# Kernel tuning notes

Hardware: AMD Instinct MI355X
Metric: run time of the kernel (lower is better)

## Reference

```python
import jax, jax.numpy as jnp
import numpy as np

_MIN_BLOCK_KV = 32


def setup_inputs() -> dict:
    key = jax.random.key(0)
    k0, k1, k2, k3 = jax.random.split(key, 4)
    B, H, HKV, D, T, S = 32, 32, 8, 128, 2048, 8
    pool = B * T
    q = jax.random.normal(k0, (B, H, D), dtype=jnp.float32)
    k_buffer = jax.random.normal(k1, (pool, HKV, D), dtype=jnp.float32)
    v_buffer = jax.random.normal(k2, (pool, HKV, D), dtype=jnp.float32)
    # uniform contexts: request b owns tokens [b*T, (b+1)*T) of the pool, in permuted (paged) order
    kv_indptr = (jnp.arange(B + 1, dtype=jnp.int32) * T)
    kv_indices = jax.random.permutation(k3, pool).astype(jnp.int32)
    num_kv_splits = jnp.full((B,), S, dtype=jnp.int32)
    return {"q": q, "k_buffer": k_buffer, "v_buffer": v_buffer,
            "kv_indptr": kv_indptr, "kv_indices": kv_indices,
            "num_kv_splits": num_kv_splits}


def reference(q, k_buffer, v_buffer, kv_indptr, kv_indices, num_kv_splits):
    # Paged KV-cache decode attention, stage 1 (split-KV partial softmax).
    B, H, D = q.shape
    HKV = k_buffer.shape[1]
    Lv = v_buffer.shape[-1]
    G = H // HKV                       # GQA group size
    sm_scale = 1.0 / (D ** 0.5)        # Model default (sm_scale=None)
    logit_cap = 0.0                    # Model default -> capping disabled

    seq_lens = kv_indptr[1:] - kv_indptr[:-1]          # [B]
    T = kv_indices.shape[0] // B                       # max context len (uniform setup)
    S = int(jnp.max(num_kv_splits))                    # max_kv_splits (eager, as in torch code)

    pos = jnp.arange(T, dtype=jnp.int32)               # [T]
    valid = pos[None, :] < seq_lens[:, None]           # [B,T]
    # gather KV pool locations per (batch, position); clamp OOB positions
    gidx = kv_indptr[:-1, None] + jnp.minimum(pos[None, :], seq_lens[:, None] - 1)
    kv_loc = kv_indices[gidx]                          # [B,T]
    k_g = k_buffer[kv_loc]                             # [B,T,HKV,D]
    v_g = v_buffer[kv_loc]                             # [B,T,HKV,Lv]

    qr = q.reshape(B, HKV, G, D)
    qk = jnp.einsum('bkgd,btkd->bkgt', qr, k_g) * sm_scale   # [B,HKV,G,T]
    if logit_cap > 0:
        qk = logit_cap * jnp.tanh(qk / logit_cap)

    # split assignment: kv_len_per_split = cdiv(cdiv(seq_len, splits), MIN) * MIN
    cdiv = lambda a, b: (a + b - 1) // b
    kv_len_per_split = cdiv(cdiv(seq_lens, num_kv_splits), _MIN_BLOCK_KV) * _MIN_BLOCK_KV  # [B]
    split_id = pos[None, :] // kv_len_per_split[:, None]      # [B,T]
    split_mask = (split_id[:, None, :] == jnp.arange(S, dtype=jnp.int32)[None, :, None]) \
                 & valid[:, None, :]                          # [B,S,T]

    neg_inf = jnp.float32(-jnp.inf)
    masked = jnp.where(split_mask[:, None, None, :, :], qk[:, :, :, None, :], neg_inf)  # [B,HKV,G,S,T]
    m = jnp.max(masked, axis=-1)                               # [B,HKV,G,S]
    m_safe = jnp.where(jnp.isfinite(m), m, 0.0)                # guard empty splits
    p = jnp.exp(masked - m_safe[..., None])                    # [B,HKV,G,S,T]
    p = jnp.where(split_mask[:, None, None, :, :], p, 0.0)
    e_sum = jnp.sum(p, axis=-1)                                # [B,HKV,G,S]
    acc = jnp.einsum('bkgst,btkv->bkgsv', p, v_g)              # [B,HKV,G,S,Lv]

    att_out = (acc / e_sum[..., None]).reshape(B, H, S, Lv)
    att_lse = (m + jnp.log(e_sum)).reshape(B, H, S)
    return att_out, att_lse
```

## Files before the change

### kernel.cpp

```cpp
#include <hip/hip_runtime.h>
#include <math.h>


namespace {
constexpr int kB = 32;
constexpr int kH = 32;
constexpr int kHKV = 8;
constexpr int kD = 128;
constexpr int kG = kH / kHKV;
constexpr int kS = 8;
constexpr int kMinBlockKV = 32;
}

__global__ __launch_bounds__(256, 8) void decode_split_kernel(
    const float* __restrict__ q,
    const float* __restrict__ k_buffer,
    const float* __restrict__ v_buffer,
    const int* __restrict__ kv_indptr,
    const int* __restrict__ kv_indices,
    const int* __restrict__ num_kv_splits,
    float* __restrict__ att_out,
    float* __restrict__ att_lse)
{
    const int bid = blockIdx.x;
    const int s  = bid % kS;
    const int kh = (bid / kS) % kHKV;
    const int b  = bid / (kS * kHKV);

    const int tid  = threadIdx.x;
    const int wave = tid >> 6;
    const int lane = tid & 63;

    const int ptr0    = kv_indptr[b];
    const int seq_len = kv_indptr[b + 1] - ptr0;
    const int splits  = num_kv_splits[b];
    const int per     = (seq_len + splits - 1) / splits;
    const int lps     = ((per + kMinBlockKV - 1) / kMinBlockKV) * kMinBlockKV;
    const int t0 = s * lps;
    const int t1 = min(t0 + lps, seq_len);

    const float sm_scale = 0.08838834764831845f;

    float2 qv[kG];
    const float* qbase = q + ((size_t)b * kH + (size_t)kh * kG) * kD + lane * 2;
    #pragma unroll
    for (int g = 0; g < kG; ++g) {
        float2 t = *(const float2*)(qbase + (size_t)g * kD);
        qv[g].x = t.x * sm_scale;
        qv[g].y = t.y * sm_scale;
    }

    float  l[kG]   = {0.f, 0.f, 0.f, 0.f};
    float2 acc[kG];
    #pragma unroll
    for (int g = 0; g < kG; ++g) acc[g] = make_float2(0.f, 0.f);

    for (int base = t0 + wave * 64; base < t1; base += 256) {
        const int nt = min(64, t1 - base);
        int my_loc = 0;
        if (lane < nt) my_loc = kv_indices[ptr0 + base + lane];

        for (int tt = 0; tt < nt; ++tt) {
            const int loc = __shfl(my_loc, tt);
            const float* krow = k_buffer + ((size_t)loc * kHKV + kh) * kD + lane * 2;
            const float* vrow = v_buffer + ((size_t)loc * kHKV + kh) * kD + lane * 2;
            const float2 kk = *(const float2*)krow;
            const float2 vv = *(const float2*)vrow;

            float dot[kG];
            #pragma unroll
            for (int g = 0; g < kG; ++g)
                dot[g] = qv[g].x * kk.x + qv[g].y * kk.y;
            #pragma unroll
            for (int m = 32; m >= 1; m >>= 1) {
                #pragma unroll
                for (int g = 0; g < kG; ++g)
                    dot[g] += __shfl_xor(dot[g], m);
            }
            #pragma unroll
            for (int g = 0; g < kG; ++g) {
                const float p = __expf(dot[g]);
                l[g] += p;
                acc[g].x += p * vv.x;
                acc[g].y += p * vv.y;
            }
        }
    }

    __shared__ float s_acc[4][kG][kD];
    __shared__ float s_l[4][kG];
    #pragma unroll
    for (int g = 0; g < kG; ++g)
        *(float2*)&s_acc[wave][g][lane * 2] = acc[g];
    if (lane == 0) {
        #pragma unroll
        for (int g = 0; g < kG; ++g) s_l[wave][g] = l[g];
    }
    __syncthreads();

    const int g = tid >> 6;
    const int d = (tid & 63) * 2;
    float a0 = 0.f, a1 = 0.f, ls = 0.f;
    #pragma unroll
    for (int w = 0; w < 4; ++w) {
        a0 += s_acc[w][g][d];
        a1 += s_acc[w][g][d + 1];
        ls += s_l[w][g];
    }
    const float inv = 1.0f / ls;
    const size_t hidx = (size_t)b * kH + (size_t)kh * kG + g;
    float* outp = att_out + (hidx * kS + s) * kD + d;
    outp[0] = a0 * inv;
    outp[1] = a1 * inv;
    if ((tid & 63) == 0)
        att_lse[hidx * kS + s] = logf(ls);
}

extern "C" void kernel_launch(void* const* d_in, const int* in_sizes, int n_in,
                              void* d_out, int out_size, void* d_ws, size_t ws_size,
                              hipStream_t stream) {
    const float* q             = (const float*)d_in[0];
    const float* k_buffer      = (const float*)d_in[1];
    const float* v_buffer      = (const float*)d_in[2];
    const int*   kv_indptr     = (const int*)d_in[3];
    const int*   kv_indices    = (const int*)d_in[4];
    const int*   num_kv_splits = (const int*)d_in[5];

    float* att_out = (float*)d_out;
    float* att_lse = att_out + (size_t)kB * kH * kS * kD;

    dim3 grid(kB * kHKV * kS);
    decode_split_kernel<<<grid, 256, 0, stream>>>(
        q, k_buffer, v_buffer, kv_indptr, kv_indices, num_kv_splits,
        att_out, att_lse);
}
```

Before: 555.5 us.

## Process four tokens per wave with float4 loads and register prefetch

```diff
diff --git a/kernel.cpp b/kernel.cpp
--- a/kernel.cpp
+++ b/kernel.cpp
@@ -12,7 +12,7 @@
 constexpr int kMinBlockKV = 32;
 }
 
-__global__ __launch_bounds__(256, 8) void decode_split_kernel(
+__global__ __launch_bounds__(256, 4) void decode_split_kernel(
     const float* __restrict__ q,
     const float* __restrict__ k_buffer,
     const float* __restrict__ v_buffer,
@@ -30,6 +30,8 @@
     const int tid  = threadIdx.x;
     const int wave = tid >> 6;
     const int lane = tid & 63;
+    const int tg   = lane >> 4;
+    const int li   = lane & 15;
 
     const int ptr0    = kv_indptr[b];
     const int seq_len = kv_indptr[b + 1] - ptr0;
@@ -41,77 +43,136 @@
 
     const float sm_scale = 0.08838834764831845f;
 
-    float2 qv[kG];
-    const float* qbase = q + ((size_t)b * kH + (size_t)kh * kG) * kD + lane * 2;
+    float4 q0[kG], q1[kG];
+    const float* qb = q + ((size_t)b * kH + (size_t)kh * kG) * kD;
     #pragma unroll
     for (int g = 0; g < kG; ++g) {
-        float2 t = *(const float2*)(qbase + (size_t)g * kD);
-        qv[g].x = t.x * sm_scale;
-        qv[g].y = t.y * sm_scale;
+        float4 a = *(const float4*)(qb + (size_t)g * kD + li * 4);
+        float4 c = *(const float4*)(qb + (size_t)g * kD + 64 + li * 4);
+        q0[g] = make_float4(a.x * sm_scale, a.y * sm_scale, a.z * sm_scale, a.w * sm_scale);
+        q1[g] = make_float4(c.x * sm_scale, c.y * sm_scale, c.z * sm_scale, c.w * sm_scale);
     }
 
-    float  l[kG]   = {0.f, 0.f, 0.f, 0.f};
-    float2 acc[kG];
+    float  l[kG] = {0.f, 0.f, 0.f, 0.f};
+    float4 a0[kG], a1[kG];
     #pragma unroll
-    for (int g = 0; g < kG; ++g) acc[g] = make_float2(0.f, 0.f);
+    for (int g = 0; g < kG; ++g) {
+        a0[g] = make_float4(0.f, 0.f, 0.f, 0.f);
+        a1[g] = make_float4(0.f, 0.f, 0.f, 0.f);
+    }
 
     for (int base = t0 + wave * 64; base < t1; base += 256) {
         const int nt = min(64, t1 - base);
         int my_loc = 0;
         if (lane < nt) my_loc = kv_indices[ptr0 + base + lane];
+        const int ng = (nt + 3) >> 2;
 
-        for (int tt = 0; tt < nt; ++tt) {
-            const int loc = __shfl(my_loc, tt);
-            const float* krow = k_buffer + ((size_t)loc * kHKV + kh) * kD + lane * 2;
-            const float* vrow = v_buffer + ((size_t)loc * kHKV + kh) * kD + lane * 2;
-            const float2 kk = *(const float2*)krow;
-            const float2 vv = *(const float2*)vrow;
+        int loc = __shfl(my_loc, min(tg, nt - 1));
+        const float* kb = k_buffer + ((size_t)loc * kHKV + kh) * kD;
+        const float* vb = v_buffer + ((size_t)loc * kHKV + kh) * kD;
+        float4 ck0 = *(const float4*)(kb + li * 4);
+        float4 ck1 = *(const float4*)(kb + 64 + li * 4);
+        float4 cv0 = *(const float4*)(vb + li * 4);
+        float4 cv1 = *(const float4*)(vb + 64 + li * 4);
+
+        for (int ig = 0; ig < ng; ++ig) {
+            float4 nk0, nk1, nv0, nv1;
+            const bool have_next = (ig + 1 < ng);
+            if (have_next) {
+                const int idx = (ig + 1) * 4 + tg;
+                const int loc2 = __shfl(my_loc, min(idx, nt - 1));
+                const float* kb2 = k_buffer + ((size_t)loc2 * kHKV + kh) * kD;
+                const float* vb2 = v_buffer + ((size_t)loc2 * kHKV + kh) * kD;
+                nk0 = *(const float4*)(kb2 + li * 4);
+                nk1 = *(const float4*)(kb2 + 64 + li * 4);
+                nv0 = *(const float4*)(vb2 + li * 4);
+                nv1 = *(const float4*)(vb2 + 64 + li * 4);
+            }
 
             float dot[kG];
             #pragma unroll
-            for (int g = 0; g < kG; ++g)
-                dot[g] = qv[g].x * kk.x + qv[g].y * kk.y;
+            for (int g = 0; g < kG; ++g) {
+                float d = q0[g].x * ck0.x;
+                d = fmaf(q0[g].y, ck0.y, d);
+                d = fmaf(q0[g].z, ck0.z, d);
+                d = fmaf(q0[g].w, ck0.w, d);
+                d = fmaf(q1[g].x, ck1.x, d);
+                d = fmaf(q1[g].y, ck1.y, d);
+                d = fmaf(q1[g].z, ck1.z, d);
+                d = fmaf(q1[g].w, ck1.w, d);
+                dot[g] = d;
+            }
             #pragma unroll
-            for (int m = 32; m >= 1; m >>= 1) {
+            for (int m = 1; m <= 8; m <<= 1) {
                 #pragma unroll
                 for (int g = 0; g < kG; ++g)
                     dot[g] += __shfl_xor(dot[g], m);
             }
+
+            const bool valid = (ig * 4 + tg) < nt;
             #pragma unroll
             for (int g = 0; g < kG; ++g) {
-                const float p = __expf(dot[g]);
+                const float p = valid ? __expf(dot[g]) : 0.f;
                 l[g] += p;
-                acc[g].x += p * vv.x;
-                acc[g].y += p * vv.y;
+                a0[g].x = fmaf(p, cv0.x, a0[g].x);
+                a0[g].y = fmaf(p, cv0.y, a0[g].y);
+                a0[g].z = fmaf(p, cv0.z, a0[g].z);
+                a0[g].w = fmaf(p, cv0.w, a0[g].w);
+                a1[g].x = fmaf(p, cv1.x, a1[g].x);
+                a1[g].y = fmaf(p, cv1.y, a1[g].y);
+                a1[g].z = fmaf(p, cv1.z, a1[g].z);
+                a1[g].w = fmaf(p, cv1.w, a1[g].w);
             }
+
+            if (have_next) { ck0 = nk0; ck1 = nk1; cv0 = nv0; cv1 = nv1; }
+        }
+    }
+
+    #pragma unroll
+    for (int m = 16; m <= 32; m <<= 1) {
+        #pragma unroll
+        for (int g = 0; g < kG; ++g) {
+            a0[g].x += __shfl_xor(a0[g].x, m);
+            a0[g].y += __shfl_xor(a0[g].y, m);
+            a0[g].z += __shfl_xor(a0[g].z, m);
+            a0[g].w += __shfl_xor(a0[g].w, m);
+            a1[g].x += __shfl_xor(a1[g].x, m);
+            a1[g].y += __shfl_xor(a1[g].y, m);
+            a1[g].z += __shfl_xor(a1[g].z, m);
+            a1[g].w += __shfl_xor(a1[g].w, m);
+            l[g] += __shfl_xor(l[g], m);
         }
     }
 
     __shared__ float s_acc[4][kG][kD];
     __shared__ float s_l[4][kG];
-    #pragma unroll
-    for (int g = 0; g < kG; ++g)
-        *(float2*)&s_acc[wave][g][lane * 2] = acc[g];
-    if (lane == 0) {
+    if (tg == 0) {
         #pragma unroll
-        for (int g = 0; g < kG; ++g) s_l[wave][g] = l[g];
+        for (int g = 0; g < kG; ++g) {
+            *(float4*)&s_acc[wave][g][li * 4]      = a0[g];
+            *(float4*)&s_acc[wave][g][64 + li * 4] = a1[g];
+        }
+        if (li == 0) {
+            #pragma unroll
+            for (int g = 0; g < kG; ++g) s_l[wave][g] = l[g];
+        }
     }
     __syncthreads();
 
     const int g = tid >> 6;
     const int d = (tid & 63) * 2;
-    float a0 = 0.f, a1 = 0.f, ls = 0.f;
+    float o0 = 0.f, o1 = 0.f, ls = 0.f;
     #pragma unroll
     for (int w = 0; w < 4; ++w) {
-        a0 += s_acc[w][g][d];
-        a1 += s_acc[w][g][d + 1];
+        o0 += s_acc[w][g][d];
+        o1 += s_acc[w][g][d + 1];
         ls += s_l[w][g];
     }
     const float inv = 1.0f / ls;
     const size_t hidx = (size_t)b * kH + (size_t)kh * kG + g;
     float* outp = att_out + (hidx * kS + s) * kD + d;
-    outp[0] = a0 * inv;
-    outp[1] = a1 * inv;
+    outp[0] = o0 * inv;
+    outp[1] = o1 * inv;
     if ((tid & 63) == 0)
         att_lse[hidx * kS + s] = logf(ls);
 }
```

Measured after the change: 538.9 us. 3.0% less time.
